# Kernel optimization log

Hardware: AMD Instinct MI355X
Metric: run time of the kernel (lower is better)

Reference implementation:

```python
import jax, jax.numpy as jnp
import numpy as np

B, S, H, NREL = 4, 512, 256, 99


def setup_inputs() -> dict:
    key = jax.random.key(0)
    ks = jax.random.split(key, 6)
    return {
        "queries": jax.random.normal(ks[0], (B, S, H), dtype=jnp.float32),
        "keys": jax.random.normal(ks[1], (B, S, H), dtype=jnp.float32),
        "relations": jax.random.randint(ks[2], (B, S, S), 0, NREL, dtype=jnp.int64),
        "Wq": jax.random.normal(ks[3], (H, H), dtype=jnp.float32) * 0.02,
        "bq": jnp.zeros((H,), dtype=jnp.float32),
        "Wk": jax.random.normal(ks[4], (H, H), dtype=jnp.float32) * 0.02,
        "bk": jnp.zeros((H,), dtype=jnp.float32),
        "rel_emb": jax.random.normal(ks[5], (NREL, H), dtype=jnp.float32) * 0.02,
    }


def reference(queries, keys, relations, Wq, bq, Wk, bk, rel_emb):
    # Linear projections (torch Linear: x @ W.T + b)
    q = queries @ Wq.T + bq        # [B, Sq, H]
    k = keys @ Wk.T + bk           # [B, Sk, H]
    r = rel_emb[relations]         # [B, Sq, Sk, H]

    # single head: qk^T + q . r^T, scaled
    qk = jnp.einsum("bqd,bkd->bqk", q, k)       # [B, Sq, Sk]
    qr = jnp.einsum("bqd,bqkd->bqk", q, r)      # [B, Sq, Sk]
    scale = 1.0 / jnp.sqrt(jnp.asarray(q.shape[-1], q.dtype))
    logits = (qk + qr) * scale
    return jax.nn.softmax(logits, axis=-1)       # squeezed head dim -> [B, Sq, Sk]
```

## Files before the change

kernel.cpp:

```cpp
#include <hip/hip_runtime.h>

typedef __attribute__((ext_vector_type(8))) short bf8;
typedef __attribute__((ext_vector_type(4))) float f4;

static __device__ __forceinline__ short bfr(float x) {
    union { float f; unsigned u; } v; v.f = x;
    return (short)((v.u + 0x7FFF + ((v.u >> 16) & 1)) >> 16);
}
static __device__ __forceinline__ float bf2f(short s) {
    union { float f; unsigned u; } v; v.u = ((unsigned)(unsigned short)s) << 16;
    return v.f;
}
static __device__ __forceinline__ bf8 pack8(float4 a, float4 b) {
    bf8 r;
    r[0] = bfr(a.x); r[1] = bfr(a.y); r[2] = bfr(a.z); r[3] = bfr(a.w);
    r[4] = bfr(b.x); r[5] = bfr(b.y); r[6] = bfr(b.z); r[7] = bfr(b.w);
    return r;
}

__global__ __launch_bounds__(512) void fused_attn(
    const float* __restrict__ queries, const float* __restrict__ keys,
    const int* __restrict__ relations, const float* __restrict__ Wq,
    const float* __restrict__ bq, const float* __restrict__ Wk,
    const float* __restrict__ bk, const float* __restrict__ rel_emb,
    float* __restrict__ out)
{
    __shared__ short q_l[8][264];
    __shared__ short t_l[8][264];
    __shared__ float qr_l[16][112];
    __shared__ float red_m[16][8];
    __shared__ float red_s[16][8];
    __shared__ float qbk_l[8];

    int blk = blockIdx.x;
    int b = blk >> 6;
    int i0 = (blk & 63) * 8;
    int gi0 = b * 512 + i0;
    int w = threadIdx.x >> 6;
    int lane = threadIdx.x & 63;
    int n15 = lane & 15, quad = lane >> 4;

    const int* rb = relations + (gi0 + (quad & 1) * 4) * 512 + w * 64 + n15;
    int rv[4][4];
#pragma unroll
    for (int reg = 0; reg < 4; reg++)
#pragma unroll
        for (int nt = 0; nt < 4; nt++)
            rv[nt][reg] = rb[reg * 512 + nt * 16];

    f4 z = {0.f, 0.f, 0.f, 0.f};

    int arow = gi0 + (n15 & 7);
    bf8 aq[8];
#pragma unroll
    for (int kk = 0; kk < 8; kk++) {
        const float4* ap = (const float4*)(queries + arow * 256 + kk * 32 + quad * 8);
        aq[kk] = pack8(ap[0], ap[1]);
    }
    {
        f4 cq[2] = {z, z};
#pragma unroll
        for (int nt = 0; nt < 2; nt++) {
            int col = w * 32 + nt * 16 + n15;
            const float* wqr = Wq + col * 256 + quad * 8;
#pragma unroll
            for (int kk = 0; kk < 8; kk++) {
                const float4* bp = (const float4*)(wqr + kk * 32);
                cq[nt] = __builtin_amdgcn_mfma_f32_16x16x32_bf16(aq[kk], pack8(bp[0], bp[1]),
                                                                 cq[nt], 0, 0, 0);
            }
        }
        if (quad < 2) {
#pragma unroll
            for (int nt = 0; nt < 2; nt++) {
                int col = w * 32 + nt * 16 + n15;
                float bv = bq[col];
#pragma unroll
                for (int reg = 0; reg < 4; reg++)
                    q_l[quad * 4 + reg][col] = bfr(cq[nt][reg] + bv);
            }
        }
    }
    __syncthreads();

    bf8 aQ[8];
#pragma unroll
    for (int kk = 0; kk < 8; kk++)
        aQ[kk] = *(const bf8*)&q_l[n15 & 7][kk * 32 + quad * 8];

    {
        f4 ct[2] = {z, z};
#pragma unroll
        for (int nt = 0; nt < 2; nt++) {
            int h = w * 32 + nt * 16 + n15;
#pragma unroll
            for (int kk = 0; kk < 8; kk++) {
                const float* wp = Wk + (kk * 32 + quad * 8) * 256 + h;
                bf8 bf_;
#pragma unroll
                for (int j = 0; j < 8; j++) bf_[j] = bfr(wp[j * 256]);
                ct[nt] = __builtin_amdgcn_mfma_f32_16x16x32_bf16(aQ[kk], bf_, ct[nt], 0, 0, 0);
            }
        }
        if (quad < 2) {
#pragma unroll
            for (int nt = 0; nt < 2; nt++) {
                int h = w * 32 + nt * 16 + n15;
#pragma unroll
                for (int reg = 0; reg < 4; reg++)
                    t_l[quad * 4 + reg][h] = bfr(ct[nt][reg]);
            }
        }
    }

    {
        const short* qp = &q_l[w][lane * 4];
        float4 bkv = *(const float4*)(bk + lane * 4);
        float a0 = bf2f(qp[0]) * bkv.x + bf2f(qp[1]) * bkv.y +
                   bf2f(qp[2]) * bkv.z + bf2f(qp[3]) * bkv.w;
#pragma unroll
        for (int d = 1; d <= 32; d <<= 1) a0 += __shfl_xor(a0, d, 64);
        if (lane == 0) qbk_l[w] = a0;
    }
    __syncthreads();

    bf8 aT[8];
#pragma unroll
    for (int kk = 0; kk < 8; kk++)
        aT[kk] = *(const bf8*)&t_l[n15 & 7][kk * 32 + quad * 8];

    f4 c[4] = {z, z, z, z};
#pragma unroll
    for (int nt = 0; nt < 4; nt++) {
        int krow = b * 512 + w * 64 + nt * 16 + n15;
        const float* kr = keys + krow * 256 + quad * 8;
#pragma unroll
        for (int kk = 0; kk < 8; kk++) {
            const float4* kp = (const float4*)(kr + kk * 32);
            c[nt] = __builtin_amdgcn_mfma_f32_16x16x32_bf16(aT[kk], pack8(kp[0], kp[1]),
                                                            c[nt], 0, 0, 0);
        }
    }

    if (w < 7) {
        f4 cr = z;
        int rrow = w * 16 + n15;
        bool valid = rrow < 99;
        const float* rp = rel_emb + (valid ? rrow : 0) * 256 + quad * 8;
#pragma unroll
        for (int kk = 0; kk < 8; kk++) {
            const float4* rpp = (const float4*)(rp + kk * 32);
            float4 x0 = rpp[0], x1 = rpp[1];
            if (!valid) { x0 = make_float4(0.f, 0.f, 0.f, 0.f); x1 = x0; }
            cr = __builtin_amdgcn_mfma_f32_16x16x32_bf16(aQ[kk], pack8(x0, x1), cr, 0, 0, 0);
        }
#pragma unroll
        for (int reg = 0; reg < 4; reg++)
            qr_l[quad * 4 + reg][rrow] = cr[reg];
    }
    __syncthreads();

    const float scale = 0.0625f;
    float lg[4][4];
#pragma unroll
    for (int nt = 0; nt < 4; nt++)
#pragma unroll
        for (int reg = 0; reg < 4; reg++)
            lg[nt][reg] = (c[nt][reg] + qr_l[quad * 4 + reg][rv[nt][reg]] +
                           qbk_l[(quad & 1) * 4 + reg]) * scale;

    float pm[4];
#pragma unroll
    for (int reg = 0; reg < 4; reg++) {
        float m = fmaxf(fmaxf(lg[0][reg], lg[1][reg]), fmaxf(lg[2][reg], lg[3][reg]));
#pragma unroll
        for (int d = 1; d <= 8; d <<= 1) m = fmaxf(m, __shfl_xor(m, d, 64));
        pm[reg] = m;
    }
    if (n15 == 0)
#pragma unroll
        for (int reg = 0; reg < 4; reg++) red_m[quad * 4 + reg][w] = pm[reg];
    __syncthreads();
    float M[4];
#pragma unroll
    for (int reg = 0; reg < 4; reg++) {
        f4 a0 = *(const f4*)&red_m[quad * 4 + reg][0];
        f4 a1 = *(const f4*)&red_m[quad * 4 + reg][4];
        M[reg] = fmaxf(fmaxf(fmaxf(a0[0], a0[1]), fmaxf(a0[2], a0[3])),
                       fmaxf(fmaxf(a1[0], a1[1]), fmaxf(a1[2], a1[3])));
    }

    float ps[4];
#pragma unroll
    for (int reg = 0; reg < 4; reg++) {
        float s = 0.f;
#pragma unroll
        for (int nt = 0; nt < 4; nt++) {
            float e = __expf(lg[nt][reg] - M[reg]);
            lg[nt][reg] = e;
            s += e;
        }
#pragma unroll
        for (int d = 1; d <= 8; d <<= 1) s += __shfl_xor(s, d, 64);
        ps[reg] = s;
    }
    if (n15 == 0)
#pragma unroll
        for (int reg = 0; reg < 4; reg++) red_s[quad * 4 + reg][w] = ps[reg];
    __syncthreads();
    float inv[4];
#pragma unroll
    for (int reg = 0; reg < 4; reg++) {
        f4 a0 = *(const f4*)&red_s[quad * 4 + reg][0];
        f4 a1 = *(const f4*)&red_s[quad * 4 + reg][4];
        inv[reg] = 1.f / (a0[0] + a0[1] + a0[2] + a0[3] + a1[0] + a1[1] + a1[2] + a1[3]);
    }

    if (quad < 2) {
        float* ob = out + (gi0 + quad * 4) * 512 + w * 64 + n15;
#pragma unroll
        for (int reg = 0; reg < 4; reg++)
#pragma unroll
            for (int nt = 0; nt < 4; nt++)
                ob[reg * 512 + nt * 16] = lg[nt][reg] * inv[reg];
    }
}

extern "C" void kernel_launch(void* const* d_in, const int* in_sizes, int n_in,
                              void* d_out, int out_size, void* d_ws, size_t ws_size,
                              hipStream_t stream) {
    const float* queries = (const float*)d_in[0];
    const float* keys = (const float*)d_in[1];
    const int* relations = (const int*)d_in[2];
    const float* Wq = (const float*)d_in[3];
    const float* bq = (const float*)d_in[4];
    const float* Wk = (const float*)d_in[5];
    const float* bk = (const float*)d_in[6];
    const float* rel_emb = (const float*)d_in[7];
    float* out = (float*)d_out;

    hipLaunchKernelGGL(fused_attn, dim3(256), dim3(512), 0, stream,
                       queries, keys, relations, Wq, bq, Wk, bk, rel_emb, out);
}
```

Measured before the change: 107.6 us.

## Double block to 1024 threads, halving per-wave projection and key work

Grows the workgroup from 8 to 16 waves so each wave computes one 16-column tile of the Q and T projections and 32 key columns instead of two tiles and 64 columns. The Wk fragment loads are hoisted to kernel start so they overlap the Q projection, and the softmax reductions now span 16 partial values per row. This is meant to raise latency hiding and shorten each wave's serial MFMA chain. The cost is more threads per block, larger cross-wave reductions, and a tighter register budget under launch_bounds(1024,4).

```diff
diff --git a/kernel.cpp b/kernel.cpp
--- a/kernel.cpp
+++ b/kernel.cpp
@@ -18,7 +18,7 @@
     return r;
 }
 
-__global__ __launch_bounds__(512) void fused_attn(
+__global__ __launch_bounds__(1024, 4) void fused_attn(
     const float* __restrict__ queries, const float* __restrict__ keys,
     const int* __restrict__ relations, const float* __restrict__ Wq,
     const float* __restrict__ bq, const float* __restrict__ Wk,
@@ -28,8 +28,8 @@
     __shared__ short q_l[8][264];
     __shared__ short t_l[8][264];
     __shared__ float qr_l[16][112];
-    __shared__ float red_m[16][8];
-    __shared__ float red_s[16][8];
+    __shared__ float red_m[16][16];
+    __shared__ float red_s[16][16];
     __shared__ float qbk_l[8];
 
     int blk = blockIdx.x;
@@ -39,14 +39,27 @@
     int w = threadIdx.x >> 6;
     int lane = threadIdx.x & 63;
     int n15 = lane & 15, quad = lane >> 4;
-
-    const int* rb = relations + (gi0 + (quad & 1) * 4) * 512 + w * 64 + n15;
-    int rv[4][4];
+    int j0 = w * 32;
+
+    const int* rb = relations + (gi0 + (quad & 1) * 4) * 512 + j0 + n15;
+    int rv[2][4];
 #pragma unroll
     for (int reg = 0; reg < 4; reg++)
 #pragma unroll
-        for (int nt = 0; nt < 4; nt++)
+        for (int nt = 0; nt < 2; nt++)
             rv[nt][reg] = rb[reg * 512 + nt * 16];
+
+    int h = w * 16 + n15;
+    bf8 wkfr[8];
+#pragma unroll
+    for (int kk = 0; kk < 8; kk++) {
+        const float* wp = Wk + (kk * 32 + quad * 8) * 256 + h;
+        float t0[8];
+#pragma unroll
+        for (int j = 0; j < 8; j++) t0[j] = wp[j * 256];
+#pragma unroll
+        for (int j = 0; j < 8; j++) wkfr[kk][j] = bfr(t0[j]);
+    }
 
     f4 z = {0.f, 0.f, 0.f, 0.f};
 
@@ -58,27 +71,20 @@
         aq[kk] = pack8(ap[0], ap[1]);
     }
     {
-        f4 cq[2] = {z, z};
-#pragma unroll
-        for (int nt = 0; nt < 2; nt++) {
-            int col = w * 32 + nt * 16 + n15;
-            const float* wqr = Wq + col * 256 + quad * 8;
-#pragma unroll
-            for (int kk = 0; kk < 8; kk++) {
-                const float4* bp = (const float4*)(wqr + kk * 32);
-                cq[nt] = __builtin_amdgcn_mfma_f32_16x16x32_bf16(aq[kk], pack8(bp[0], bp[1]),
-                                                                 cq[nt], 0, 0, 0);
-            }
+        f4 cq = z;
+        int colA = w * 16 + n15;
+        const float* wqr = Wq + colA * 256 + quad * 8;
+#pragma unroll
+        for (int kk = 0; kk < 8; kk++) {
+            const float4* bp = (const float4*)(wqr + kk * 32);
+            cq = __builtin_amdgcn_mfma_f32_16x16x32_bf16(aq[kk], pack8(bp[0], bp[1]),
+                                                         cq, 0, 0, 0);
         }
         if (quad < 2) {
-#pragma unroll
-            for (int nt = 0; nt < 2; nt++) {
-                int col = w * 32 + nt * 16 + n15;
-                float bv = bq[col];
-#pragma unroll
-                for (int reg = 0; reg < 4; reg++)
-                    q_l[quad * 4 + reg][col] = bfr(cq[nt][reg] + bv);
-            }
+            float bv = bq[colA];
+#pragma unroll
+            for (int reg = 0; reg < 4; reg++)
+                q_l[quad * 4 + reg][colA] = bfr(cq[reg] + bv);
         }
     }
     __syncthreads();
@@ -89,31 +95,18 @@
         aQ[kk] = *(const bf8*)&q_l[n15 & 7][kk * 32 + quad * 8];
 
     {
-        f4 ct[2] = {z, z};
-#pragma unroll
-        for (int nt = 0; nt < 2; nt++) {
-            int h = w * 32 + nt * 16 + n15;
-#pragma unroll
-            for (int kk = 0; kk < 8; kk++) {
-                const float* wp = Wk + (kk * 32 + quad * 8) * 256 + h;
-                bf8 bf_;
-#pragma unroll
-                for (int j = 0; j < 8; j++) bf_[j] = bfr(wp[j * 256]);
-                ct[nt] = __builtin_amdgcn_mfma_f32_16x16x32_bf16(aQ[kk], bf_, ct[nt], 0, 0, 0);
-            }
-        }
+        f4 ct = z;
+#pragma unroll
+        for (int kk = 0; kk < 8; kk++)
+            ct = __builtin_amdgcn_mfma_f32_16x16x32_bf16(aQ[kk], wkfr[kk], ct, 0, 0, 0);
         if (quad < 2) {
 #pragma unroll
-            for (int nt = 0; nt < 2; nt++) {
-                int h = w * 32 + nt * 16 + n15;
-#pragma unroll
-                for (int reg = 0; reg < 4; reg++)
-                    t_l[quad * 4 + reg][h] = bfr(ct[nt][reg]);
-            }
-        }
-    }
-
-    {
+            for (int reg = 0; reg < 4; reg++)
+                t_l[quad * 4 + reg][h] = bfr(ct[reg]);
+        }
+    }
+
+    if (w < 8) {
         const short* qp = &q_l[w][lane * 4];
         float4 bkv = *(const float4*)(bk + lane * 4);
         float a0 = bf2f(qp[0]) * bkv.x + bf2f(qp[1]) * bkv.y +
@@ -129,10 +122,10 @@
     for (int kk = 0; kk < 8; kk++)
         aT[kk] = *(const bf8*)&t_l[n15 & 7][kk * 32 + quad * 8];
 
-    f4 c[4] = {z, z, z, z};
-#pragma unroll
-    for (int nt = 0; nt < 4; nt++) {
-        int krow = b * 512 + w * 64 + nt * 16 + n15;
+    f4 c[2] = {z, z};
+#pragma unroll
+    for (int nt = 0; nt < 2; nt++) {
+        int krow = b * 512 + j0 + nt * 16 + n15;
         const float* kr = keys + krow * 256 + quad * 8;
 #pragma unroll
         for (int kk = 0; kk < 8; kk++) {
@@ -161,9 +154,9 @@
     __syncthreads();
 
     const float scale = 0.0625f;
-    float lg[4][4];
-#pragma unroll
-    for (int nt = 0; nt < 4; nt++)
+    float lg[2][4];
+#pragma unroll
+    for (int nt = 0; nt < 2; nt++)
 #pragma unroll
         for (int reg = 0; reg < 4; reg++)
             lg[nt][reg] = (c[nt][reg] + qr_l[quad * 4 + reg][rv[nt][reg]] +
@@ -172,7 +165,7 @@
     float pm[4];
 #pragma unroll
     for (int reg = 0; reg < 4; reg++) {
-        float m = fmaxf(fmaxf(lg[0][reg], lg[1][reg]), fmaxf(lg[2][reg], lg[3][reg]));
+        float m = fmaxf(lg[0][reg], lg[1][reg]);
 #pragma unroll
         for (int d = 1; d <= 8; d <<= 1) m = fmaxf(m, __shfl_xor(m, d, 64));
         pm[reg] = m;
@@ -186,8 +179,13 @@
     for (int reg = 0; reg < 4; reg++) {
         f4 a0 = *(const f4*)&red_m[quad * 4 + reg][0];
         f4 a1 = *(const f4*)&red_m[quad * 4 + reg][4];
-        M[reg] = fmaxf(fmaxf(fmaxf(a0[0], a0[1]), fmaxf(a0[2], a0[3])),
-                       fmaxf(fmaxf(a1[0], a1[1]), fmaxf(a1[2], a1[3])));
+        f4 a2 = *(const f4*)&red_m[quad * 4 + reg][8];
+        f4 a3 = *(const f4*)&red_m[quad * 4 + reg][12];
+        float m0 = fmaxf(fmaxf(a0[0], a0[1]), fmaxf(a0[2], a0[3]));
+        float m1 = fmaxf(fmaxf(a1[0], a1[1]), fmaxf(a1[2], a1[3]));
+        float m2 = fmaxf(fmaxf(a2[0], a2[1]), fmaxf(a2[2], a2[3]));
+        float m3 = fmaxf(fmaxf(a3[0], a3[1]), fmaxf(a3[2], a3[3]));
+        M[reg] = fmaxf(fmaxf(m0, m1), fmaxf(m2, m3));
     }
 
     float ps[4];
@@ -195,7 +193,7 @@
     for (int reg = 0; reg < 4; reg++) {
         float s = 0.f;
 #pragma unroll
-        for (int nt = 0; nt < 4; nt++) {
+        for (int nt = 0; nt < 2; nt++) {
             float e = __expf(lg[nt][reg] - M[reg]);
             lg[nt][reg] = e;
             s += e;
@@ -213,15 +211,18 @@
     for (int reg = 0; reg < 4; reg++) {
         f4 a0 = *(const f4*)&red_s[quad * 4 + reg][0];
         f4 a1 = *(const f4*)&red_s[quad * 4 + reg][4];
-        inv[reg] = 1.f / (a0[0] + a0[1] + a0[2] + a0[3] + a1[0] + a1[1] + a1[2] + a1[3]);
+        f4 a2 = *(const f4*)&red_s[quad * 4 + reg][8];
+        f4 a3 = *(const f4*)&red_s[quad * 4 + reg][12];
+        inv[reg] = 1.f / (a0[0] + a0[1] + a0[2] + a0[3] + a1[0] + a1[1] + a1[2] + a1[3] +
+                          a2[0] + a2[1] + a2[2] + a2[3] + a3[0] + a3[1] + a3[2] + a3[3]);
     }
 
     if (quad < 2) {
-        float* ob = out + (gi0 + quad * 4) * 512 + w * 64 + n15;
+        float* ob = out + (gi0 + quad * 4) * 512 + j0 + n15;
 #pragma unroll
         for (int reg = 0; reg < 4; reg++)
 #pragma unroll
-            for (int nt = 0; nt < 4; nt++)
+            for (int nt = 0; nt < 2; nt++)
                 ob[reg * 512 + nt * 16] = lg[nt][reg] * inv[reg];
     }
 }
@@ -239,6 +240,6 @@
     const float* rel_emb = (const float*)d_in[7];
     float* out = (float*)d_out;
 
-    hipLaunchKernelGGL(fused_attn, dim3(256), dim3(512), 0, stream,
+    hipLaunchKernelGGL(fused_attn, dim3(256), dim3(1024), 0, stream,
                        queries, keys, relations, Wq, bq, Wk, bk, rel_emb, out);
 }
```

After: 112.9 us. 4.9% more time.
